# Kernel optimization log

Hardware: AMD Instinct MI355X
Metric: run time of the kernel (lower is better)

Reference implementation:

```python
import jax, jax.numpy as jnp
import numpy as np

FEATURE_MAPS = [38, 19, 10, 5, 3, 1]
NUM_ANCHORS = [4, 6, 6, 6, 4, 4]
SCALES = (0.2, 0.9)
RATIOS = np.array([1.0, 1.0, 2.0, 3.0, 0.5, 1.0 / 3.0])
BACKGROUND_ID = 0
EPS = 1e-6


def _generate_anchors():
    """Replicates AnchorManager._generate_anchors: order is (i, j, k)."""
    all_anchors = []
    for size, n in zip(FEATURE_MAPS, NUM_ANCHORS):
        scales = np.linspace(SCALES[0], SCALES[1], n)
        ratios = RATIOS[:n]
        rs = np.sqrt(ratios)
        w = scales * rs          # [n]
        h = scales / rs          # [n]
        cy = (np.arange(size) + 0.5) / size  # i -> rows (varies slowest)
        cx = (np.arange(size) + 0.5) / size  # j -> cols
        grid = np.zeros((size, size, n, 4), dtype=np.float64)
        grid[..., 0] = cx[None, :, None]
        grid[..., 1] = cy[:, None, None]
        grid[..., 2] = w[None, None, :]
        grid[..., 3] = h[None, None, :]
        all_anchors.append(grid.reshape(-1, 4))
    return np.concatenate(all_anchors).astype(np.float32)  # [A, 4] cxcywh


def _cxcywh_to_xyxy(b):
    cxy, wh = b[..., :2], b[..., 2:]
    return jnp.concatenate([cxy - wh / 2, cxy + wh / 2], axis=-1)


def _xyxy_to_cxcywh(b):
    xy1, xy2 = b[..., :2], b[..., 2:]
    return jnp.concatenate([(xy1 + xy2) / 2, xy2 - xy1], axis=-1)


def setup_inputs() -> dict:
    key = jax.random.key(0)
    k1, k2, k3 = jax.random.split(key, 3)
    B, N = 64, 100
    # valid normalized xyxy gt boxes
    xy = jax.random.uniform(k1, (B, N, 2), dtype=jnp.float32) * 0.8
    wh = jax.random.uniform(k2, (B, N, 2), dtype=jnp.float32) * 0.19 + 0.01
    gt_boxes = jnp.concatenate([xy, xy + wh], axis=-1)
    gt_labels = jax.random.randint(k3, (B, N), 1, 81, dtype=jnp.int64 if jax.config.jax_enable_x64 else jnp.int32).astype(jnp.int32)
    anchors_cxcywh = jnp.asarray(_generate_anchors())          # [A, 4]
    anchors_xyxy = _cxcywh_to_xyxy(anchors_cxcywh)             # [A, 4]
    return {
        "gt_labels": gt_labels,
        "gt_boxes": gt_boxes,
        "anchors_cxcywh": anchors_cxcywh,
        "anchors_xyxy": anchors_xyxy,
    }


def _iou(anchors_xyxy, gt_boxes):
    # anchors_xyxy: [A,4], gt_boxes: [B,N,4] -> iou [B,A,N]
    a = anchors_xyxy[None, :, None, :]   # [1,A,1,4]
    g = gt_boxes[:, None, :, :]          # [B,1,N,4]
    lt = jnp.maximum(a[..., :2], g[..., :2])
    rb = jnp.minimum(a[..., 2:], g[..., 2:])
    wh = jnp.clip(rb - lt, 0.0)
    inter = wh[..., 0] * wh[..., 1]
    area_a = (a[..., 2] - a[..., 0]) * (a[..., 3] - a[..., 1])
    area_g = (g[..., 2] - g[..., 0]) * (g[..., 3] - g[..., 1])
    return (inter / (area_a + area_g - inter)).astype(jnp.float32)


def reference(gt_labels, gt_boxes, anchors_cxcywh, anchors_xyxy):
    B, N = gt_boxes.shape[0], gt_boxes.shape[1]
    A = anchors_cxcywh.shape[0]

    gt_boxes_coco = _xyxy_to_cxcywh(gt_boxes)                  # [B,N,4]
    ious = _iou(anchors_xyxy, gt_boxes)                        # [B,A,N]

    anchors_gt = jnp.max(ious, axis=-1)                        # [B,A]
    anchors_gt_idx = jnp.argmax(ious, axis=-1)                 # [B,A]
    gt_anchors_idx = jnp.argmax(ious, axis=-2)                 # [B,N] best anchor per gt

    # force-match: each gt claims its best anchor
    b_idx = jnp.arange(B)[:, None]
    range_n = jnp.broadcast_to(jnp.arange(N), (B, N))
    anchors_gt_idx = anchors_gt_idx.at[b_idx, gt_anchors_idx].set(range_n)
    anchors_gt = anchors_gt.at[b_idx, gt_anchors_idx].set(2.0)

    pos_mask = anchors_gt > 0.5                                # [B,A]

    matched_gtb = jnp.take_along_axis(gt_boxes_coco, anchors_gt_idx[..., None], axis=1)  # [B,A,4]
    matched_labels = jnp.take_along_axis(gt_labels, anchors_gt_idx, axis=1)              # [B,A]
    encoded_labels = jnp.where(pos_mask, matched_labels, BACKGROUND_ID)

    anc = anchors_cxcywh[None]                                 # [1,A,4]
    enc_cxy = (matched_gtb[..., :2] - anc[..., :2]) / anc[..., 2:]
    enc_wh = jnp.log((matched_gtb[..., 2:] + EPS) / (anc[..., 2:] + EPS))
    encoded = jnp.concatenate([enc_cxy, enc_wh], axis=-1)      # [B,A,4]

    return encoded_labels, encoded, pos_mask
```

## Files before the change

kernel.cpp:

```cpp
#include <hip/hip_runtime.h>
#include <math.h>

#pragma clang fp contract(off)


#define AA 8732
#define NN 100
#define BB 64
#define EPS_F 1e-6f
#define OVR_FLAG 0x10000
#define POS_BIT  0x8000
#define DEFL 0.9999995f

__constant__ int FM_SIZE[6] = {38, 19, 10, 5, 3, 1};
__constant__ int FM_NF[6]   = {4, 6, 6, 6, 4, 4};
__constant__ int FM_OFF[6]  = {0, 5776, 7942, 8542, 8692, 8728};

__device__ __forceinline__ void geom(const float4 axy, const float4 g,
                                     float area_a, float ag,
                                     float& inter, float& uni) {
    float ltx = fmaxf(axy.x, g.x);
    float lty = fmaxf(axy.y, g.y);
    float rbx = fminf(axy.z, g.z);
    float rby = fminf(axy.w, g.w);
    float w = fmaxf(rbx - ltx, 0.0f);
    float h = fmaxf(rby - lty, 0.0f);
    inter = w * h;
    uni = area_a + ag - inter;
}

__global__ void prior_kernel(const float4* __restrict__ gt_boxes,
                             const float4* __restrict__ anchors_xyxy,
                             float* __restrict__ prior,
                             unsigned long long* __restrict__ colmax) {
    const int b = blockIdx.x;
    const int n = threadIdx.x;
    if (n >= NN) return;
    float4 g = gt_boxes[b * NN + n];
    float ag = (g.z - g.x) * (g.w - g.y);
    float cx = (g.x + g.z) * 0.5f;
    float cy = (g.y + g.w) * 0.5f;
    float best = 0.0f;
    for (int f = 0; f < 6; f++) {
        int s = FM_SIZE[f];
        int j = (int)(cx * (float)s); j = j < s - 1 ? j : s - 1;
        int i = (int)(cy * (float)s); i = i < s - 1 ? i : s - 1;
        int base = FM_OFF[f] + (i * s + j) * FM_NF[f];
        for (int k = 0; k < FM_NF[f]; k++) {
            float4 an = anchors_xyxy[base + k];
            float area_a = (an.z - an.x) * (an.w - an.y);
            float inter, uni;
            geom(an, g, area_a, ag, inter, uni);
            best = fmaxf(best, inter * __builtin_amdgcn_rcpf(uni));
        }
    }
    float defl = best * DEFL;
    prior[b * NN + n] = defl;
    colmax[b * NN + n] = ((unsigned long long)__float_as_uint(defl)) << 32;
}

template <int N0, int N1>
__device__ __forceinline__ void passChunk(
        const float4 axy, const float area_a, const unsigned lowkey,
        const int b, const int tid,
        const float4* __restrict__ sg,
        float2* sac,
        unsigned long long* __restrict__ colmax,
        float& rt, unsigned& rm)
{
    #pragma unroll 4
    for (int n = N0; n < N1; n++) {
        float4 g = sg[n];
        float2 aw = sac[n];
        float inter, uni;
        geom(axy, g, area_a, aw.x, inter, uni);
        float qa = inter * __builtin_amdgcn_rcpf(uni);
        bool r = (qa > 0.0f) && (qa >= rt);
        rt = fmaxf(rt, qa * DEFL);
        rm |= (r ? 1u : 0u) << (n - N0);
        if (__any((int)(qa >= aw.y))) {
            float iou = inter / uni;
            bool cc = (qa >= aw.y);
            unsigned long long p = cc
                ? ((((unsigned long long)__float_as_uint(iou)) << 32) |
                   (unsigned long long)lowkey) : 0ull;
            #pragma unroll
            for (int off = 32; off > 0; off >>= 1) {
                unsigned long long o = __shfl_xor(p, off);
                p = o > p ? o : p;
            }
            if ((tid & 63) == 0 && p != 0ull) {
                atomicMax(colmax + b * NN + n, p);
                atomicMax((unsigned*)&sac[n].y,
                    __float_as_uint(__uint_as_float((unsigned)(p >> 32)) * DEFL));
            }
        }
    }
}

__global__ __launch_bounds__(256) void iou_pass_kernel(
        const float4* __restrict__ gt_boxes,
        const float4* __restrict__ anchors_xyxy,
        const float* __restrict__ prior,
        unsigned long long* __restrict__ colmax,
        int* __restrict__ out_slot)
{
    const int b = blockIdx.y;
    const int tid = threadIdx.x;
    const int a = blockIdx.x * 256 + tid;
    const bool valid = (a < AA);
    const int ac = valid ? a : (AA - 1);

    __shared__ float4 sg[NN];
    __shared__ float2 sac[NN];

    if (tid < NN) {
        float4 g = gt_boxes[b * NN + tid];
        sg[tid] = g;
        sac[tid] = make_float2((g.z - g.x) * (g.w - g.y),
                               prior[b * NN + tid]);
    }
    __syncthreads();

    const float4 axy = anchors_xyxy[ac];
    const float area_a = (axy.z - axy.x) * (axy.w - axy.y);
    const unsigned lowkey = (unsigned)(AA - ac);

    float rt = 0.0f;
    unsigned rm0 = 0, rm1 = 0, rm2 = 0, rm3 = 0;
    passChunk<0, 32>(axy, area_a, lowkey, b, tid, sg, sac, colmax, rt, rm0);
    passChunk<32, 64>(axy, area_a, lowkey, b, tid, sg, sac, colmax, rt, rm1);
    passChunk<64, 96>(axy, area_a, lowkey, b, tid, sg, sac, colmax, rt, rm2);
    passChunk<96, NN>(axy, area_a, lowkey, b, tid, sg, sac, colmax, rt, rm3);

    float bv = 0.0f;
    int bi = 0;
    unsigned rms[4] = {rm0, rm1, rm2, rm3};
    #pragma unroll
    for (int h = 0; h < 4; h++) {
        unsigned m = rms[h];
        const int nb = h * 32;
        while (m) {
            int n = __builtin_ctz(m) + nb;
            m &= m - 1;
            float inter, uni;
            geom(axy, sg[n], area_a, sac[n].x, inter, uni);
            float qa = inter * __builtin_amdgcn_rcpf(uni);
            if (qa > 0.0f && qa >= rt) {
                float iou = inter / uni;
                if (iou > bv) { bv = iou; bi = n; }
            }
        }
    }

    if (valid) {
        out_slot[(size_t)b * AA + a] = bi | (bv > 0.5f ? POS_BIT : 0);
    }
}

__global__ void scatter_kernel(const unsigned long long* __restrict__ colmax,
                               int* __restrict__ out_slot) {
    const int b = blockIdx.x;
    const int n = threadIdx.x;
    if (n < NN) {
        unsigned long long v = colmax[b * NN + n];
        unsigned low = (unsigned)(v & 0xFFFFFFFFull);
        if (low >= 1u && low <= (unsigned)AA) {
            int idx = AA - (int)low;
            atomicMax(&out_slot[(size_t)b * AA + idx], OVR_FLAG + n);
        }
    }
}

__global__ __launch_bounds__(256) void encode_kernel(
        const int* __restrict__ gt_labels,
        const float4* __restrict__ gt_boxes,
        const float4* __restrict__ anchors_cxcywh,
        float* __restrict__ out)
{
    const int b = blockIdx.y;
    const int tid = threadIdx.x;
    const int a = blockIdx.x * 256 + tid;

    __shared__ float4 sg[NN];
    __shared__ int    slab[NN];
    if (tid < NN) {
        sg[tid]   = gt_boxes[b * NN + tid];
        slab[tid] = gt_labels[b * NN + tid];
    }
    __syncthreads();
    if (a >= AA) return;

    const size_t BA = (size_t)BB * AA;
    const size_t base = (size_t)b * AA + a;

    int s = ((const int*)(out + 5 * BA))[base];

    int idx; bool pos;
    if (s >= OVR_FLAG) { idx = s - OVR_FLAG;  pos = true; }
    else               { idx = s & 0x7FFF;    pos = (s & POS_BIT) != 0; }

    const float4 g = sg[idx];
    const float gcx = (g.x + g.z) * 0.5f;
    const float gcy = (g.y + g.w) * 0.5f;
    const float gw  = g.z - g.x;
    const float gh  = g.w - g.y;

    const float4 anc = anchors_cxcywh[a];
    const float ecx = (gcx - anc.x) / anc.z;
    const float ecy = (gcy - anc.y) / anc.w;
    const float ew  = logf((gw + EPS_F) / (anc.z + EPS_F));
    const float eh  = logf((gh + EPS_F) / (anc.w + EPS_F));

    out[base] = pos ? (float)slab[idx] : 0.0f;
    ((float4*)(out + BA))[base] = make_float4(ecx, ecy, ew, eh);
    out[5 * BA + base] = pos ? 1.0f : 0.0f;
}

extern "C" void kernel_launch(void* const* d_in, const int* in_sizes, int n_in,
                              void* d_out, int out_size, void* d_ws, size_t ws_size,
                              hipStream_t stream) {
    const int*    gt_labels    = (const int*)d_in[0];
    const float4* gt_boxes     = (const float4*)d_in[1];
    const float4* anchors_cxcy = (const float4*)d_in[2];
    const float4* anchors_xyxy = (const float4*)d_in[3];
    float* out = (float*)d_out;

    const size_t BA = (size_t)BB * AA;
    unsigned long long* colmax = (unsigned long long*)(out + BA);
    int* slot = (int*)(out + 5 * BA);
    float* prior = (float*)d_ws;

    prior_kernel<<<BB, 128, 0, stream>>>(gt_boxes, anchors_xyxy, prior, colmax);

    dim3 grid((AA + 255) / 256, BB);
    iou_pass_kernel<<<grid, 256, 0, stream>>>(gt_boxes, anchors_xyxy, prior,
                                              colmax, slot);
    scatter_kernel<<<BB, 128, 0, stream>>>(colmax, slot);
    encode_kernel<<<grid, 256, 0, stream>>>(gt_labels, gt_boxes, anchors_cxcy,
                                            out);
}
```

Baseline: 130.6 us.

## Read gt boxes via uniform global loads and widen prior anchor search

```diff
diff --git a/kernel.cpp b/kernel.cpp
--- a/kernel.cpp
+++ b/kernel.cpp
@@ -31,7 +31,7 @@
 
 __global__ void prior_kernel(const float4* __restrict__ gt_boxes,
                              const float4* __restrict__ anchors_xyxy,
-                             float* __restrict__ prior,
+                             float4* __restrict__ gtab,
                              unsigned long long* __restrict__ colmax) {
     const int b = blockIdx.x;
     const int n = threadIdx.x;
@@ -43,19 +43,29 @@
     float best = 0.0f;
     for (int f = 0; f < 6; f++) {
         int s = FM_SIZE[f];
-        int j = (int)(cx * (float)s); j = j < s - 1 ? j : s - 1;
-        int i = (int)(cy * (float)s); i = i < s - 1 ? i : s - 1;
-        int base = FM_OFF[f] + (i * s + j) * FM_NF[f];
-        for (int k = 0; k < FM_NF[f]; k++) {
-            float4 an = anchors_xyxy[base + k];
-            float area_a = (an.z - an.x) * (an.w - an.y);
-            float inter, uni;
-            geom(an, g, area_a, ag, inter, uni);
-            best = fmaxf(best, inter * __builtin_amdgcn_rcpf(uni));
+        int j0 = (int)(cx * (float)s); j0 = j0 < s - 1 ? j0 : s - 1;
+        int i0 = (int)(cy * (float)s); i0 = i0 < s - 1 ? i0 : s - 1;
+        int rad = (f < 2) ? 1 : 0;
+        for (int di = -rad; di <= rad; di++) {
+            int i = i0 + di;
+            if (i < 0 || i >= s) continue;
+            for (int dj = -rad; dj <= rad; dj++) {
+                int j = j0 + dj;
+                if (j < 0 || j >= s) continue;
+                int base = FM_OFF[f] + (i * s + j) * FM_NF[f];
+                for (int k = 0; k < FM_NF[f]; k++) {
+                    float4 an = anchors_xyxy[base + k];
+                    float area_a = (an.z - an.x) * (an.w - an.y);
+                    float inter, uni;
+                    geom(an, g, area_a, ag, inter, uni);
+                    best = fmaxf(best, inter * __builtin_amdgcn_rcpf(uni));
+                }
+            }
         }
     }
     float defl = best * DEFL;
-    prior[b * NN + n] = defl;
+    gtab[(b * NN + n) * 2 + 0] = g;
+    gtab[(b * NN + n) * 2 + 1] = make_float4(ag, defl, 0.0f, 0.0f);
     colmax[b * NN + n] = ((unsigned long long)__float_as_uint(defl)) << 32;
 }
 
@@ -63,24 +73,25 @@
 __device__ __forceinline__ void passChunk(
         const float4 axy, const float area_a, const unsigned lowkey,
         const int b, const int tid,
-        const float4* __restrict__ sg,
-        float2* sac,
+        const float4* __restrict__ gtab,
+        float* scurf,
         unsigned long long* __restrict__ colmax,
         float& rt, unsigned& rm)
 {
     #pragma unroll 4
     for (int n = N0; n < N1; n++) {
-        float4 g = sg[n];
-        float2 aw = sac[n];
+        float4 g  = gtab[(b * NN + n) * 2 + 0];
+        float  ag = gtab[(b * NN + n) * 2 + 1].x;
         float inter, uni;
-        geom(axy, g, area_a, aw.x, inter, uni);
+        geom(axy, g, area_a, ag, inter, uni);
         float qa = inter * __builtin_amdgcn_rcpf(uni);
         bool r = (qa > 0.0f) && (qa >= rt);
         rt = fmaxf(rt, qa * DEFL);
         rm |= (r ? 1u : 0u) << (n - N0);
-        if (__any((int)(qa >= aw.y))) {
+        float cf = scurf[n];
+        if (__any((int)(qa >= cf))) {
             float iou = inter / uni;
-            bool cc = (qa >= aw.y);
+            bool cc = (qa >= cf);
             unsigned long long p = cc
                 ? ((((unsigned long long)__float_as_uint(iou)) << 32) |
                    (unsigned long long)lowkey) : 0ull;
@@ -91,7 +102,7 @@
             }
             if ((tid & 63) == 0 && p != 0ull) {
                 atomicMax(colmax + b * NN + n, p);
-                atomicMax((unsigned*)&sac[n].y,
+                atomicMax((unsigned*)&scurf[n],
                     __float_as_uint(__uint_as_float((unsigned)(p >> 32)) * DEFL));
             }
         }
@@ -99,9 +110,8 @@
 }
 
 __global__ __launch_bounds__(256) void iou_pass_kernel(
-        const float4* __restrict__ gt_boxes,
+        const float4* __restrict__ gtab,
         const float4* __restrict__ anchors_xyxy,
-        const float* __restrict__ prior,
         unsigned long long* __restrict__ colmax,
         int* __restrict__ out_slot)
 {
@@ -111,15 +121,9 @@
     const bool valid = (a < AA);
     const int ac = valid ? a : (AA - 1);
 
-    __shared__ float4 sg[NN];
-    __shared__ float2 sac[NN];
-
-    if (tid < NN) {
-        float4 g = gt_boxes[b * NN + tid];
-        sg[tid] = g;
-        sac[tid] = make_float2((g.z - g.x) * (g.w - g.y),
-                               prior[b * NN + tid]);
-    }
+    __shared__ float scurf[NN];
+
+    if (tid < NN) scurf[tid] = gtab[(b * NN + tid) * 2 + 1].y;
     __syncthreads();
 
     const float4 axy = anchors_xyxy[ac];
@@ -128,10 +132,10 @@
 
     float rt = 0.0f;
     unsigned rm0 = 0, rm1 = 0, rm2 = 0, rm3 = 0;
-    passChunk<0, 32>(axy, area_a, lowkey, b, tid, sg, sac, colmax, rt, rm0);
-    passChunk<32, 64>(axy, area_a, lowkey, b, tid, sg, sac, colmax, rt, rm1);
-    passChunk<64, 96>(axy, area_a, lowkey, b, tid, sg, sac, colmax, rt, rm2);
-    passChunk<96, NN>(axy, area_a, lowkey, b, tid, sg, sac, colmax, rt, rm3);
+    passChunk<0, 32>(axy, area_a, lowkey, b, tid, gtab, scurf, colmax, rt, rm0);
+    passChunk<32, 64>(axy, area_a, lowkey, b, tid, gtab, scurf, colmax, rt, rm1);
+    passChunk<64, 96>(axy, area_a, lowkey, b, tid, gtab, scurf, colmax, rt, rm2);
+    passChunk<96, NN>(axy, area_a, lowkey, b, tid, gtab, scurf, colmax, rt, rm3);
 
     float bv = 0.0f;
     int bi = 0;
@@ -143,8 +147,10 @@
         while (m) {
             int n = __builtin_ctz(m) + nb;
             m &= m - 1;
+            float4 g  = gtab[(b * NN + n) * 2 + 0];
+            float  ag = gtab[(b * NN + n) * 2 + 1].x;
             float inter, uni;
-            geom(axy, sg[n], area_a, sac[n].x, inter, uni);
+            geom(axy, g, area_a, ag, inter, uni);
             float qa = inter * __builtin_amdgcn_rcpf(uni);
             if (qa > 0.0f && qa >= rt) {
                 float iou = inter / uni;
@@ -229,13 +235,16 @@
     const size_t BA = (size_t)BB * AA;
     unsigned long long* colmax = (unsigned long long*)(out + BA);
     int* slot = (int*)(out + 5 * BA);
-    float* prior = (float*)d_ws;
-
-    prior_kernel<<<BB, 128, 0, stream>>>(gt_boxes, anchors_xyxy, prior, colmax);
+
+    const size_t gtab_bytes = (size_t)BB * NN * 2 * sizeof(float4);
+    float4* gtab = (ws_size >= gtab_bytes)
+        ? (float4*)d_ws
+        : (float4*)(out + BA + (size_t)BB * NN * 2);
+
+    prior_kernel<<<BB, 128, 0, stream>>>(gt_boxes, anchors_xyxy, gtab, colmax);
 
     dim3 grid((AA + 255) / 256, BB);
-    iou_pass_kernel<<<grid, 256, 0, stream>>>(gt_boxes, anchors_xyxy, prior,
-                                              colmax, slot);
+    iou_pass_kernel<<<grid, 256, 0, stream>>>(gtab, anchors_xyxy, colmax, slot);
     scatter_kernel<<<BB, 128, 0, stream>>>(colmax, slot);
     encode_kernel<<<grid, 256, 0, stream>>>(gt_labels, gt_boxes, anchors_cxcy,
                                             out);
```

After: 148.3 us. 13.5% more time.

## Fuse encoding into IoU pass, defer column-max atomics, parallelize prior search

Applied to the files above, without the earlier changes.

```diff
diff --git a/kernel.cpp b/kernel.cpp
--- a/kernel.cpp
+++ b/kernel.cpp
@@ -10,7 +10,8 @@
 #define EPS_F 1e-6f
 #define OVR_FLAG 0x10000
 #define POS_BIT  0x8000
-#define DEFL 0.9999995f
+#define DEFL  0.9999995f
+#define FDEFL 0.9999996f
 
 __constant__ int FM_SIZE[6] = {38, 19, 10, 5, 3, 1};
 __constant__ int FM_NF[6]   = {4, 6, 6, 6, 4, 4};
@@ -29,80 +30,97 @@
     uni = area_a + ag - inter;
 }
 
-__global__ void prior_kernel(const float4* __restrict__ gt_boxes,
-                             const float4* __restrict__ anchors_xyxy,
-                             float* __restrict__ prior,
-                             unsigned long long* __restrict__ colmax) {
-    const int b = blockIdx.x;
-    const int n = threadIdx.x;
-    if (n >= NN) return;
+__device__ __forceinline__ float4 enc_box(const float4 g, const float4 anc) {
+    float gcx = (g.x + g.z) * 0.5f;
+    float gcy = (g.y + g.w) * 0.5f;
+    float gw  = g.z - g.x;
+    float gh  = g.w - g.y;
+    return make_float4((gcx - anc.x) / anc.z,
+                       (gcy - anc.y) / anc.w,
+                       logf((gw + EPS_F) / (anc.z + EPS_F)),
+                       logf((gh + EPS_F) / (anc.w + EPS_F)));
+}
+
+__device__ __forceinline__ int prior_cand(int c, float cx, float cy) {
+    int f, k, di, dj;
+    if (c < 36)       { f = 0; k = c & 3;  int cl = c >> 2;      di = cl / 3 - 1; dj = cl % 3 - 1; }
+    else if (c < 90)  { int t = c - 36; f = 1; k = t % 6; int cl = t / 6; di = cl / 3 - 1; dj = cl % 3 - 1; }
+    else if (c < 96)  { f = 2; k = c - 90;  di = 0; dj = 0; }
+    else if (c < 102) { f = 3; k = c - 96;  di = 0; dj = 0; }
+    else if (c < 106) { f = 4; k = c - 102; di = 0; dj = 0; }
+    else              { f = 5; k = c - 106; di = 0; dj = 0; }
+    int s = FM_SIZE[f];
+    int j = (int)(cx * (float)s); j = j < s - 1 ? j : s - 1;
+    int i = (int)(cy * (float)s); i = i < s - 1 ? i : s - 1;
+    j += dj; i += di;
+    if (j < 0 || j >= s || i < 0 || i >= s) return -1;
+    return FM_OFF[f] + (i * s + j) * FM_NF[f] + k;
+}
+
+__global__ __launch_bounds__(256) void prior_kernel(
+        const float4* __restrict__ gt_boxes,
+        const float4* __restrict__ anchors_xyxy,
+        unsigned long long* __restrict__ colmax) {
+    const int b = blockIdx.y;
+    const int n = blockIdx.x * 4 + (threadIdx.x >> 6);
+    const int lane = threadIdx.x & 63;
     float4 g = gt_boxes[b * NN + n];
     float ag = (g.z - g.x) * (g.w - g.y);
     float cx = (g.x + g.z) * 0.5f;
     float cy = (g.y + g.w) * 0.5f;
     float best = 0.0f;
-    for (int f = 0; f < 6; f++) {
-        int s = FM_SIZE[f];
-        int j = (int)(cx * (float)s); j = j < s - 1 ? j : s - 1;
-        int i = (int)(cy * (float)s); i = i < s - 1 ? i : s - 1;
-        int base = FM_OFF[f] + (i * s + j) * FM_NF[f];
-        for (int k = 0; k < FM_NF[f]; k++) {
-            float4 an = anchors_xyxy[base + k];
+    for (int c = lane; c < 110; c += 64) {
+        int ai = prior_cand(c, cx, cy);
+        if (ai >= 0) {
+            float4 an = anchors_xyxy[ai];
             float area_a = (an.z - an.x) * (an.w - an.y);
             float inter, uni;
             geom(an, g, area_a, ag, inter, uni);
             best = fmaxf(best, inter * __builtin_amdgcn_rcpf(uni));
         }
     }
-    float defl = best * DEFL;
-    prior[b * NN + n] = defl;
-    colmax[b * NN + n] = ((unsigned long long)__float_as_uint(defl)) << 32;
+    #pragma unroll
+    for (int off = 32; off > 0; off >>= 1)
+        best = fmaxf(best, __shfl_xor(best, off));
+    if (lane == 0) {
+        float defl = best * DEFL;
+        colmax[b * NN + n] =
+            ((unsigned long long)__float_as_uint(defl)) << 32;
+    }
 }
 
 template <int N0, int N1>
 __device__ __forceinline__ void passChunk(
-        const float4 axy, const float area_a, const unsigned lowkey,
-        const int b, const int tid,
-        const float4* __restrict__ sg,
-        float2* sac,
-        unsigned long long* __restrict__ colmax,
-        float& rt, unsigned& rm)
+        const float4 axy, const float area_a,
+        const float4* __restrict__ sg, const float2* __restrict__ sap,
+        float& ibest, float& ubest, unsigned& rm, unsigned& cm)
 {
-    #pragma unroll 4
+    #pragma unroll
     for (int n = N0; n < N1; n++) {
         float4 g = sg[n];
-        float2 aw = sac[n];
+        float2 ar = sap[n];
         float inter, uni;
-        geom(axy, g, area_a, aw.x, inter, uni);
-        float qa = inter * __builtin_amdgcn_rcpf(uni);
-        bool r = (qa > 0.0f) && (qa >= rt);
-        rt = fmaxf(rt, qa * DEFL);
-        rm |= (r ? 1u : 0u) << (n - N0);
-        if (__any((int)(qa >= aw.y))) {
-            float iou = inter / uni;
-            bool cc = (qa >= aw.y);
-            unsigned long long p = cc
-                ? ((((unsigned long long)__float_as_uint(iou)) << 32) |
-                   (unsigned long long)lowkey) : 0ull;
-            #pragma unroll
-            for (int off = 32; off > 0; off >>= 1) {
-                unsigned long long o = __shfl_xor(p, off);
-                p = o > p ? o : p;
-            }
-            if ((tid & 63) == 0 && p != 0ull) {
-                atomicMax(colmax + b * NN + n, p);
-                atomicMax((unsigned*)&sac[n].y,
-                    __float_as_uint(__uint_as_float((unsigned)(p >> 32)) * DEFL));
-            }
-        }
-    }
-}
-
+        geom(axy, g, area_a, ar.x, inter, uni);
+        float p1 = inter * ubest;
+        float p2 = ibest * uni;
+        bool fl = (inter > 0.0f) && (p1 >= p2 * FDEFL);
+        rm |= (fl ? 1u : 0u) << (n - N0);
+        bool up = p1 > p2;
+        ibest = up ? inter : ibest;
+        ubest = up ? uni : ubest;
+        bool cf = inter >= ar.y * uni;
+        cm |= (cf ? 1u : 0u) << (n - N0);
+    }
+}
+
+template <bool FUSED>
 __global__ __launch_bounds__(256) void iou_pass_kernel(
         const float4* __restrict__ gt_boxes,
+        const int*    __restrict__ gt_labels,
         const float4* __restrict__ anchors_xyxy,
-        const float* __restrict__ prior,
+        const float4* __restrict__ anchors_cxcywh,
         unsigned long long* __restrict__ colmax,
+        float* __restrict__ out,
         int* __restrict__ out_slot)
 {
     const int b = blockIdx.y;
@@ -112,13 +130,16 @@
     const int ac = valid ? a : (AA - 1);
 
     __shared__ float4 sg[NN];
-    __shared__ float2 sac[NN];
+    __shared__ float2 sap[NN];
+    __shared__ int    slab[NN];
 
     if (tid < NN) {
         float4 g = gt_boxes[b * NN + tid];
         sg[tid] = g;
-        sac[tid] = make_float2((g.z - g.x) * (g.w - g.y),
-                               prior[b * NN + tid]);
+        unsigned hi = (unsigned)(colmax[b * NN + tid] >> 32);
+        sap[tid] = make_float2((g.z - g.x) * (g.w - g.y),
+                               __uint_as_float(hi) * DEFL);
+        if (FUSED) slab[tid] = gt_labels[b * NN + tid];
     }
     __syncthreads();
 
@@ -126,36 +147,101 @@
     const float area_a = (axy.z - axy.x) * (axy.w - axy.y);
     const unsigned lowkey = (unsigned)(AA - ac);
 
-    float rt = 0.0f;
+    float ibest = 0.0f, ubest = 1.0f;
     unsigned rm0 = 0, rm1 = 0, rm2 = 0, rm3 = 0;
-    passChunk<0, 32>(axy, area_a, lowkey, b, tid, sg, sac, colmax, rt, rm0);
-    passChunk<32, 64>(axy, area_a, lowkey, b, tid, sg, sac, colmax, rt, rm1);
-    passChunk<64, 96>(axy, area_a, lowkey, b, tid, sg, sac, colmax, rt, rm2);
-    passChunk<96, NN>(axy, area_a, lowkey, b, tid, sg, sac, colmax, rt, rm3);
+    unsigned cm0 = 0, cm1 = 0, cm2 = 0, cm3 = 0;
+    passChunk<0, 32>(axy, area_a, sg, sap, ibest, ubest, rm0, cm0);
+    passChunk<32, 64>(axy, area_a, sg, sap, ibest, ubest, rm1, cm1);
+    passChunk<64, 96>(axy, area_a, sg, sap, ibest, ubest, rm2, cm2);
+    passChunk<96, NN>(axy, area_a, sg, sap, ibest, ubest, rm3, cm3);
 
     float bv = 0.0f;
     int bi = 0;
-    unsigned rms[4] = {rm0, rm1, rm2, rm3};
-    #pragma unroll
-    for (int h = 0; h < 4; h++) {
-        unsigned m = rms[h];
-        const int nb = h * 32;
-        while (m) {
-            int n = __builtin_ctz(m) + nb;
-            m &= m - 1;
-            float inter, uni;
-            geom(axy, sg[n], area_a, sac[n].x, inter, uni);
-            float qa = inter * __builtin_amdgcn_rcpf(uni);
-            if (qa > 0.0f && qa >= rt) {
+    {
+        unsigned rms[4] = {rm0, rm1, rm2, rm3};
+        #pragma unroll
+        for (int h = 0; h < 4; h++) {
+            unsigned m = rms[h];
+            const int nb = h * 32;
+            while (m) {
+                int n = __builtin_ctz(m) + nb;
+                m &= m - 1;
+                float inter, uni;
+                geom(axy, sg[n], area_a, sap[n].x, inter, uni);
                 float iou = inter / uni;
                 if (iou > bv) { bv = iou; bi = n; }
             }
         }
     }
 
-    if (valid) {
-        out_slot[(size_t)b * AA + a] = bi | (bv > 0.5f ? POS_BIT : 0);
-    }
+    {
+        unsigned cms[4] = {cm0, cm1, cm2, cm3};
+        #pragma unroll
+        for (int h = 0; h < 4; h++) {
+            unsigned wc = cms[h];
+            #pragma unroll
+            for (int off = 32; off > 0; off >>= 1)
+                wc |= __shfl_xor(wc, off);
+            const int nb = h * 32;
+            while (wc) {
+                int n = __builtin_ctz(wc) + nb;
+                wc &= wc - 1;
+                float inter, uni;
+                geom(axy, sg[n], area_a, sap[n].x, inter, uni);
+                bool cc = inter >= sap[n].y * uni;
+                float iou = inter / uni;
+                unsigned long long p = cc
+                    ? ((((unsigned long long)__float_as_uint(iou)) << 32) |
+                       (unsigned long long)lowkey) : 0ull;
+                #pragma unroll
+                for (int off = 32; off > 0; off >>= 1) {
+                    unsigned long long o = __shfl_xor(p, off);
+                    p = o > p ? o : p;
+                }
+                if ((tid & 63) == 0 && p != 0ull)
+                    atomicMax(colmax + b * NN + n, p);
+            }
+        }
+    }
+
+    if (!valid) return;
+    const size_t BA = (size_t)BB * AA;
+    const size_t base = (size_t)b * AA + a;
+    const bool pos = bv > 0.5f;
+    if (FUSED) {
+        out[base] = pos ? (float)slab[bi] : 0.0f;
+        ((float4*)(out + BA))[base] = enc_box(sg[bi], anchors_cxcywh[a]);
+        out[5 * BA + base] = pos ? 1.0f : 0.0f;
+    } else {
+        out_slot[base] = bi | (pos ? POS_BIT : 0);
+    }
+}
+
+__global__ void override_kernel(const unsigned long long* __restrict__ colmax,
+                                const float4* __restrict__ gt_boxes,
+                                const int*    __restrict__ gt_labels,
+                                const float4* __restrict__ anchors_cxcywh,
+                                float* __restrict__ out) {
+    const int b = blockIdx.x;
+    const int n = threadIdx.x;
+    __shared__ int sa[NN];
+    int an = -1;
+    if (n < NN) {
+        unsigned long long v = colmax[b * NN + n];
+        unsigned low = (unsigned)(v & 0xFFFFFFFFull);
+        if (low >= 1u && low <= (unsigned)AA) an = AA - (int)low;
+        sa[n] = an;
+    }
+    __syncthreads();
+    if (n >= NN || an < 0) return;
+    for (int n2 = n + 1; n2 < NN; n2++)
+        if (sa[n2] == an) return;
+    const size_t BA = (size_t)BB * AA;
+    const size_t base = (size_t)b * AA + an;
+    out[base] = (float)gt_labels[b * NN + n];
+    ((float4*)(out + BA))[base] =
+        enc_box(gt_boxes[b * NN + n], anchors_cxcywh[an]);
+    out[5 * BA + base] = 1.0f;
 }
 
 __global__ void scatter_kernel(const unsigned long long* __restrict__ colmax,
@@ -176,12 +262,10 @@
         const int* __restrict__ gt_labels,
         const float4* __restrict__ gt_boxes,
         const float4* __restrict__ anchors_cxcywh,
-        float* __restrict__ out)
-{
+        float* __restrict__ out) {
     const int b = blockIdx.y;
     const int tid = threadIdx.x;
     const int a = blockIdx.x * 256 + tid;
-
     __shared__ float4 sg[NN];
     __shared__ int    slab[NN];
     if (tid < NN) {
@@ -190,30 +274,14 @@
     }
     __syncthreads();
     if (a >= AA) return;
-
     const size_t BA = (size_t)BB * AA;
     const size_t base = (size_t)b * AA + a;
-
     int s = ((const int*)(out + 5 * BA))[base];
-
     int idx; bool pos;
     if (s >= OVR_FLAG) { idx = s - OVR_FLAG;  pos = true; }
     else               { idx = s & 0x7FFF;    pos = (s & POS_BIT) != 0; }
-
-    const float4 g = sg[idx];
-    const float gcx = (g.x + g.z) * 0.5f;
-    const float gcy = (g.y + g.w) * 0.5f;
-    const float gw  = g.z - g.x;
-    const float gh  = g.w - g.y;
-
-    const float4 anc = anchors_cxcywh[a];
-    const float ecx = (gcx - anc.x) / anc.z;
-    const float ecy = (gcy - anc.y) / anc.w;
-    const float ew  = logf((gw + EPS_F) / (anc.z + EPS_F));
-    const float eh  = logf((gh + EPS_F) / (anc.w + EPS_F));
-
     out[base] = pos ? (float)slab[idx] : 0.0f;
-    ((float4*)(out + BA))[base] = make_float4(ecx, ecy, ew, eh);
+    ((float4*)(out + BA))[base] = enc_box(sg[idx], anchors_cxcywh[a]);
     out[5 * BA + base] = pos ? 1.0f : 0.0f;
 }
 
@@ -227,16 +295,27 @@
     float* out = (float*)d_out;
 
     const size_t BA = (size_t)BB * AA;
-    unsigned long long* colmax = (unsigned long long*)(out + BA);
+    const size_t colmax_bytes = (size_t)BB * NN * sizeof(unsigned long long);
+    const bool fused = (ws_size >= colmax_bytes);
+    unsigned long long* colmax = fused
+        ? (unsigned long long*)d_ws
+        : (unsigned long long*)(out + BA);
     int* slot = (int*)(out + 5 * BA);
-    float* prior = (float*)d_ws;
-
-    prior_kernel<<<BB, 128, 0, stream>>>(gt_boxes, anchors_xyxy, prior, colmax);
+
+    dim3 pgrid(25, BB);
+    prior_kernel<<<pgrid, 256, 0, stream>>>(gt_boxes, anchors_xyxy, colmax);
 
     dim3 grid((AA + 255) / 256, BB);
-    iou_pass_kernel<<<grid, 256, 0, stream>>>(gt_boxes, anchors_xyxy, prior,
-                                              colmax, slot);
-    scatter_kernel<<<BB, 128, 0, stream>>>(colmax, slot);
-    encode_kernel<<<grid, 256, 0, stream>>>(gt_labels, gt_boxes, anchors_cxcy,
-                                            out);
-}
+    if (fused) {
+        iou_pass_kernel<true><<<grid, 256, 0, stream>>>(
+            gt_boxes, gt_labels, anchors_xyxy, anchors_cxcy, colmax, out, slot);
+        override_kernel<<<BB, 128, 0, stream>>>(colmax, gt_boxes, gt_labels,
+                                                anchors_cxcy, out);
+    } else {
+        iou_pass_kernel<false><<<grid, 256, 0, stream>>>(
+            gt_boxes, gt_labels, anchors_xyxy, anchors_cxcy, colmax, out, slot);
+        scatter_kernel<<<BB, 128, 0, stream>>>(colmax, slot);
+        encode_kernel<<<grid, 256, 0, stream>>>(gt_labels, gt_boxes,
+                                                anchors_cxcy, out);
+    }
+}
```

After: 224.1 us. 71.6% more time.
